# Kernel optimization log

Measured on AMD Instinct MI355X. Metric: run time of the kernel, lower is better.

## Reference

```python
import jax, jax.numpy as jnp
import numpy as np

B, N, E = 8, 5000, 80000
NODE_IN, EDGE_IN, HIDDEN, EMBED = 32, 16, 128, 64


def setup_inputs() -> dict:
    key = jax.random.key(0)
    ks = jax.random.split(key, 20)
    g = lambda k, shape: jax.random.normal(k, shape, dtype=jnp.float32) * 0.05
    return {
        "node_x": jax.random.normal(ks[0], (B, N, NODE_IN), dtype=jnp.float32),
        "edge_attr": jax.random.normal(ks[1], (B, E, EDGE_IN), dtype=jnp.float32),
        "edge_index": jax.random.randint(ks[2], (2, E), 0, N),
        "ln_node_g": jnp.ones((NODE_IN,), jnp.float32),
        "ln_node_b": jnp.zeros((NODE_IN,), jnp.float32),
        "ln_edge_g": jnp.ones((EDGE_IN,), jnp.float32),
        "ln_edge_b": jnp.zeros((EDGE_IN,), jnp.float32),
        "gat0_W": g(ks[3], (NODE_IN, HIDDEN)),
        "gat0_We": g(ks[4], (EDGE_IN, HIDDEN)),
        "gat0_asrc": g(ks[5], (HIDDEN,)),
        "gat0_adst": g(ks[6], (HIDDEN,)),
        "gat0_ae": g(ks[7], (HIDDEN,)),
        "gat0_b": jnp.zeros((HIDDEN,), jnp.float32),
        "gat1_W": g(ks[8], (HIDDEN, EMBED)),
        "gat1_We": g(ks[9], (EDGE_IN, EMBED)),
        "gat1_asrc": g(ks[10], (EMBED,)),
        "gat1_adst": g(ks[11], (EMBED,)),
        "gat1_ae": g(ks[12], (EMBED,)),
        "gat1_b": jnp.zeros((EMBED,), jnp.float32),
        "mlp_W1": g(ks[13], (4 * EMBED + EDGE_IN, HIDDEN)),
        "mlp_b1": jnp.zeros((HIDDEN,), jnp.float32),
        "mlp_W2": g(ks[14], (HIDDEN, 1)),
        "mlp_b2": jnp.zeros((1,), jnp.float32),
    }


def _layernorm(x, g, b, eps=1e-5):
    mu = x.mean(-1, keepdims=True)
    var = ((x - mu) ** 2).mean(-1, keepdims=True)
    return (x - mu) * jax.lax.rsqrt(var + eps) * g + b


def _gat_layer(x, efeat, src, dst, W, We, asrc, adst, ae, b, nseg):
    # Single-head GATConv with edge features: attention logits from src/dst/edge projections,
    # segment-softmax over incoming edges per destination node, weighted-sum aggregation.
    h = x @ W                      # [nseg, out]
    he = efeat @ We                # [num_edges, out]
    logits = jax.nn.leaky_relu(
        (h[src] * asrc).sum(-1) + (h[dst] * adst).sum(-1) + (he * ae).sum(-1), 0.2)
    m = jax.ops.segment_max(logits, dst, num_segments=nseg)
    m = jnp.where(jnp.isfinite(m), m, 0.0)
    ex = jnp.exp(logits - m[dst])
    denom = jax.ops.segment_sum(ex, dst, num_segments=nseg)
    alpha = ex / (denom[dst] + 1e-16)
    return jax.ops.segment_sum(alpha[:, None] * h[src], dst, num_segments=nseg) + b


def reference(node_x, edge_attr, edge_index, ln_node_g, ln_node_b, ln_edge_g, ln_edge_b,
              gat0_W, gat0_We, gat0_asrc, gat0_adst, gat0_ae, gat0_b,
              gat1_W, gat1_We, gat1_asrc, gat1_adst, gat1_ae, gat1_b,
              mlp_W1, mlp_b1, mlp_W2, mlp_b2):
    nx = _layernorm(node_x, ln_node_g, ln_node_b)
    ea = _layernorm(edge_attr, ln_edge_g, ln_edge_b)
    # Batched graph: offset shared edge_index per graph.
    xf = nx.reshape(B * N, NODE_IN)
    ef = ea.reshape(B * E, EDGE_IN)
    offs = jnp.arange(B) * N
    ei = (edge_index[:, None, :] + offs[None, :, None]).reshape(2, B * E)
    src, dst = ei[0], ei[1]
    batch_vec = jnp.repeat(jnp.arange(B), N)
    # GAT encoder: layer 0 (ELU) then final projection to embed.
    h = jax.nn.elu(_gat_layer(xf, ef, src, dst, gat0_W, gat0_We, gat0_asrc, gat0_adst, gat0_ae, gat0_b, B * N))
    node_emb = _gat_layer(h, ef, src, dst, gat1_W, gat1_We, gat1_asrc, gat1_adst, gat1_ae, gat1_b, B * N)
    # Global context: concat(mean, max) pooling per graph -> [B, 2*EMBED]
    mean_pool = jax.ops.segment_sum(node_emb, batch_vec, num_segments=B) / N
    max_pool = jax.ops.segment_max(node_emb, batch_vec, num_segments=B)
    ctx = jnp.concatenate([mean_pool, max_pool], axis=-1)
    # Per-edge gather-concat + MLP
    edge_emb = jnp.concatenate([node_emb[src], node_emb[dst], ef, ctx[batch_vec[src]]], axis=-1)
    hm = jax.nn.relu(edge_emb @ mlp_W1 + mlp_b1)
    q = (hm @ mlp_W2 + mlp_b2).squeeze(-1)
    return q.reshape(B, E)
```

## Files before the change

### kernel.cpp

```cpp
#include <hip/hip_runtime.h>
#include <cmath>

#define BB 8
#define NN 5000
#define EE 80000
#define NODE_IN 32
#define EDGE_IN 16
#define HIDDEN 128
#define EMBED 64
#define BN (BB*NN)
#define BE (BB*EE)

typedef unsigned short u16;
typedef __attribute__((ext_vector_type(8))) __bf16 bf16x8;
typedef __attribute__((ext_vector_type(4))) float f32x4;

__device__ __forceinline__ float waveSum(float v){
  #pragma unroll
  for(int o=32;o;o>>=1) v += __shfl_xor(v,o);
  return v;
}
__device__ __forceinline__ float waveMax(float v){
  #pragma unroll
  for(int o=32;o;o>>=1) v = fmaxf(v,__shfl_xor(v,o));
  return v;
}
__device__ __forceinline__ int rlanei(int v, int l){
  return __builtin_amdgcn_readlane(v, l);
}
__device__ __forceinline__ float rlanef(float v, int l){
  return __uint_as_float(__builtin_amdgcn_readlane(__float_as_uint(v), l));
}
__device__ __forceinline__ unsigned pack_bf2(float a0, float a1){
  unsigned u0 = __float_as_uint(a0), u1 = __float_as_uint(a1);
  unsigned r0 = (u0 + 0x7fffu + ((u0>>16)&1u)) >> 16;
  unsigned r1 = (u1 + 0x7fffu + ((u1>>16)&1u)) & 0xffff0000u;
  return r0 | r1;
}
__device__ __forceinline__ u16 bf16r(float x){
  unsigned u = __float_as_uint(x);
  return (u16)((u + 0x7fffu + ((u>>16)&1u)) >> 16);
}
__device__ __forceinline__ float bflo(unsigned h){ return __uint_as_float(h<<16); }
__device__ __forceinline__ float bfhi(unsigned h){ return __uint_as_float(h & 0xffff0000u); }
__device__ __forceinline__ bf16x8 ld8_or_zero(const u16* p, bool pred){
  uint4 v = pred ? *(const uint4*)p : make_uint4(0u,0u,0u,0u);
  return *(bf16x8*)&v;
}

__launch_bounds__(256)
__global__ void k_prep(const float* We0, const float* ae0,
                       const float* We1, const float* ae1,
                       const float* W1g, const float* asrc1, const float* adst1,
                       const float* mlpW1,
                       float* wae, float* ws1, float* wd1,
                       u16* BT1u, u16* BT2u, u16* AT1e){
  int t = threadIdx.x;
  if(blockIdx.x == 0){
    if(t < 16){
      float a = 0.f;
      for(int k=0;k<HIDDEN;k++) a += We0[t*HIDDEN+k]*ae0[k];
      wae[t] = a;
    } else if(t < 32){
      int j = t-16;
      float a = 0.f;
      for(int k=0;k<EMBED;k++) a += We1[j*EMBED+k]*ae1[k];
      wae[16+j] = a;
    }
    if(t < 128){
      float s = 0.f, d = 0.f;
      for(int k=0;k<EMBED;k++){
        float w = W1g[t*EMBED+k];
        s += w*asrc1[k];
        d += w*adst1[k];
      }
      ws1[t] = s; wd1[t] = d;
    }
    for(int i=t; i<2048; i+=256){
      int o = i >> 4, k = i & 15;
      AT1e[o*16 + k] = bf16r(mlpW1[(128+k)*HIDDEN + o]);
    }
  } else {
    #pragma unroll
    for(int ii=0; ii<6; ii++){
      int idx = (blockIdx.x-1)*1536 + ii*256 + t;
      if(idx < 8192){
        int c = idx >> 7, k = idx & 127;
        BT1u[c*136 + k] = bf16r(W1g[k*EMBED + c]);
      } else {
        int i2 = idx - 8192;
        int d = i2 >> 6, j = i2 & 63;
        float v = (d < 128) ? mlpW1[j*HIDDEN + d] : mlpW1[(64+j)*HIDDEN + (d-128)];
        BT2u[d*72 + j] = bf16r(v);
      }
    }
  }
}

__launch_bounds__(256)
__global__ void k_node(const float* __restrict__ x, const float* __restrict__ g,
                       const float* __restrict__ bb, const float* __restrict__ W,
                       const float* __restrict__ asrc, const float* __restrict__ adst,
                       unsigned* __restrict__ H0u, float* __restrict__ S0o, float* __restrict__ D0o){
  int t = threadIdx.x;
  int w = t>>6, lane = t&63;
  float w0r[NODE_IN], w1r[NODE_IN];
  #pragma unroll
  for(int j=0;j<NODE_IN;j++){
    w0r[j] = W[j*HIDDEN + 2*lane];
    w1r[j] = W[j*HIDDEN + 2*lane + 1];
  }
  float gl = (lane<NODE_IN)? g[lane] : 0.f;
  float bl = (lane<NODE_IN)? bb[lane] : 0.f;
  float asl0 = asrc[2*lane], asl1 = asrc[2*lane+1];
  float adl0 = adst[2*lane], adl1 = adst[2*lane+1];
  for(int nb = blockIdx.x; nb < BN/4; nb += gridDim.x){
    int n = nb*4 + w;
    float xv = (lane<NODE_IN)? x[n*NODE_IN+lane] : 0.f;
    float s  = waveSum(xv);
    float s2 = waveSum(xv*xv);
    float mu = s*(1.f/NODE_IN);
    float var = s2*(1.f/NODE_IN) - mu*mu;
    float inv = 1.0f / sqrtf(var + 1e-5f);
    float nx = (lane<NODE_IN)? ((xv-mu)*inv*gl + bl) : 0.f;
    float a0=0.f, a1=0.f;
    #pragma unroll
    for(int j=0;j<NODE_IN;j++){
      float r = rlanef(nx, j);
      a0 += r*w0r[j];
      a1 += r*w1r[j];
    }
    H0u[(size_t)n*64 + lane] = pack_bf2(a0, a1);
    float sv = waveSum(a0*asl0 + a1*asl1);
    float dv = waveSum(a0*adl0 + a1*adl1);
    if(lane==0){ S0o[n]=sv; D0o[n]=dv; }
  }
}

__launch_bounds__(256)
__global__ void k_edge(const float* __restrict__ ein, const float* __restrict__ g,
                       const float* __restrict__ bb, const float* __restrict__ wae,
                       const int* __restrict__ EPOS,
                       u16* __restrict__ EAb, float* __restrict__ E0p, float* __restrict__ E1p){
  int ge = blockIdx.x*256 + threadIdx.x;
  int b = ge / EE, e = ge - b*EE;
  int gp = b*EE + EPOS[e];
  float v[EDGE_IN];
  const float4* p = (const float4*)(ein + (size_t)ge*EDGE_IN);
  float4 q0=p[0], q1=p[1], q2=p[2], q3=p[3];
  v[0]=q0.x; v[1]=q0.y; v[2]=q0.z; v[3]=q0.w;
  v[4]=q1.x; v[5]=q1.y; v[6]=q1.z; v[7]=q1.w;
  v[8]=q2.x; v[9]=q2.y; v[10]=q2.z; v[11]=q2.w;
  v[12]=q3.x; v[13]=q3.y; v[14]=q3.z; v[15]=q3.w;
  float s=0.f, s2=0.f;
  #pragma unroll
  for(int j=0;j<EDGE_IN;j++){ s += v[j]; s2 += v[j]*v[j]; }
  float mu = s*(1.f/EDGE_IN);
  float var = s2*(1.f/EDGE_IN) - mu*mu;
  float inv = 1.0f / sqrtf(var + 1e-5f);
  float e0=0.f, e1=0.f;
  #pragma unroll
  for(int j=0;j<EDGE_IN;j++){
    float nv = (v[j]-mu)*inv*g[j] + bb[j];
    v[j] = nv;
    e0 += nv*wae[j];
    e1 += nv*wae[16+j];
  }
  uint4 w0 = make_uint4(pack_bf2(v[0],v[1]), pack_bf2(v[2],v[3]),
                        pack_bf2(v[4],v[5]), pack_bf2(v[6],v[7]));
  uint4 w1 = make_uint4(pack_bf2(v[8],v[9]), pack_bf2(v[10],v[11]),
                        pack_bf2(v[12],v[13]), pack_bf2(v[14],v[15]));
  uint4* q = (uint4*)&EAb[(size_t)gp*16];
  q[0] = w0; q[1] = w1;
  E0p[gp]=e0; E1p[gp]=e1;
}

__global__ void k_count(const int* __restrict__ ei, int* __restrict__ cnt){
  int e = blockIdx.x*256 + threadIdx.x;
  if(e < EE) atomicAdd(&cnt[ei[EE+e]], 1);
}

__launch_bounds__(1024)
__global__ void k_scan(int* __restrict__ off, int* __restrict__ cur){
  __shared__ int part[1024];
  int t = threadIdx.x;
  int loc[5]; int s=0;
  int base = t*5;
  #pragma unroll
  for(int k=0;k<5;k++){ int idx=base+k; int c=(idx<NN)? cur[idx]:0; loc[k]=s; s+=c; }
  part[t]=s;
  __syncthreads();
  for(int o=1;o<1024;o<<=1){
    int v = (t>=o)? part[t-o] : 0;
    __syncthreads();
    part[t] += v;
    __syncthreads();
  }
  int pre = (t>0)? part[t-1] : 0;
  #pragma unroll
  for(int k=0;k<5;k++){
    int idx=base+k;
    if(idx<NN){ int o2 = pre+loc[k]; off[idx]=o2; cur[idx]=o2; }
  }
  if(t==0) off[NN] = EE;
}

__global__ void k_fill(const int* __restrict__ ei, int* __restrict__ cur,
                       int* __restrict__ csrc, int* __restrict__ cdst,
                       int* __restrict__ ceid, int* __restrict__ epos){
  int e = blockIdx.x*256 + threadIdx.x;
  if(e < EE){
    int d = ei[EE+e];
    int pos = atomicAdd(&cur[d], 1);
    csrc[pos] = ei[e];
    cdst[pos] = d;
    ceid[pos] = e;
    epos[e] = pos;
  }
}

__launch_bounds__(256)
__global__ void k_gat0(const unsigned* __restrict__ H0u, const float* __restrict__ S0,
                       const float* __restrict__ D0, const float* __restrict__ E0p,
                       const int* __restrict__ off, const int* __restrict__ csrc,
                       const float* __restrict__ bias,
                       const float* __restrict__ WS1, const float* __restrict__ WD1,
                       unsigned* __restrict__ HELUu, float* __restrict__ S1o, float* __restrict__ D1o){
  int t = threadIdx.x, w = t>>6, lane = t&63;
  int b = blockIdx.x & 7, c = blockIdx.x >> 3;
  int n = c*4 + w;
  int gid = b*NN + n;
  int base = off[n], deg = off[n+1]-base;
  const float* s0b = S0 + b*NN;
  const float* e0b = E0p + b*EE;
  const unsigned* h0b = H0u + (size_t)b*NN*64;
  float dv = D0[gid];
  float acc0=0.f, acc1=0.f;
  if(deg > 0){
    if(deg <= 64){
      float lg = -INFINITY; int sidx = 0;
      if(lane < deg){
        sidx = csrc[base+lane];
        float xx = s0b[sidx] + dv + e0b[base+lane];
        lg = xx>0.f ? xx : 0.2f*xx;
      }
      float m = waveMax(lg);
      float ex = (lane<deg)? __expf(lg-m) : 0.f;
      float den = waveSum(ex);
      float al = ex / (den + 1e-16f);
      int nb8 = (deg+7)>>3;
      for(int b8=0;b8<nb8;b8++){
        int i0 = b8*8;
        int ss[8]; float aa[8]; unsigned hh[8];
        #pragma unroll
        for(int kk=0;kk<8;kk++){ ss[kk]=rlanei(sidx, i0+kk); aa[kk]=rlanef(al, i0+kk); }
        #pragma unroll
        for(int kk=0;kk<8;kk++){ hh[kk]=h0b[ss[kk]*64 + lane]; }
        #pragma unroll
        for(int kk=0;kk<8;kk++){ acc0 += aa[kk]*bflo(hh[kk]); acc1 += aa[kk]*bfhi(hh[kk]); }
      }
    } else {
      float m = -INFINITY;
      for(int i=lane;i<deg;i+=64){
        float xx = s0b[csrc[base+i]] + dv + e0b[base+i];
        xx = xx>0.f ? xx : 0.2f*xx;
        m = fmaxf(m, xx);
      }
      m = waveMax(m);
      float den = 0.f;
      for(int i=lane;i<deg;i+=64){
        float xx = s0b[csrc[base+i]] + dv + e0b[base+i];
        xx = xx>0.f ? xx : 0.2f*xx;
        den += __expf(xx-m);
      }
      den = waveSum(den) + 1e-16f;
      for(int i=0;i<deg;i++){
        int s = csrc[base+i];
        float xx = s0b[s] + dv + e0b[base+i];
        xx = xx>0.f ? xx : 0.2f*xx;
        float a = __expf(xx-m)/den;
        unsigned h = h0b[s*64 + lane];
        acc0 += a*bflo(h);
        acc1 += a*bfhi(h);
      }
    }
  }
  float2 bi = *(const float2*)&bias[2*lane];
  float v0 = acc0 + bi.x;
  float v1 = acc1 + bi.y;
  v0 = v0>0.f ? v0 : (__expf(v0)-1.f);
  v1 = v1>0.f ? v1 : (__expf(v1)-1.f);
  HELUu[(size_t)gid*64 + lane] = pack_bf2(v0, v1);
  float2 wsv = *(const float2*)&WS1[2*lane];
  float2 wdv = *(const float2*)&WD1[2*lane];
  float sv1 = waveSum(v0*wsv.x + v1*wsv.y);
  float dv1 = waveSum(v0*wdv.x + v1*wdv.y);
  if(lane==0){ S1o[gid]=sv1; D1o[gid]=dv1; }
}

__launch_bounds__(256)
__global__ void k_h1(const unsigned* __restrict__ HELUu, const u16* __restrict__ BT1,
                     u16* __restrict__ H1u){
  __shared__ u16 Ald[64*136];
  __shared__ u16 Bld[64*136];
  int t = threadIdx.x;
  int n0 = blockIdx.x*64;
  #pragma unroll
  for(int ii=0; ii<4; ii++){
    int c2 = ii*256 + t;
    int r = c2 >> 4, q = c2 & 15;
    *(uint4*)&Ald[r*136 + q*8] = ((const uint4*)(HELUu + (size_t)(n0+r)*64))[q];
  }
  for(int i=t; i<1088; i+=256) ((uint4*)Bld)[i] = ((const uint4*)BT1)[i];
  __syncthreads();
  int w = t>>6, lane = t&63;
  int lo = lane & 15, hi = lane >> 4;
  f32x4 acc0 = {0.f,0.f,0.f,0.f}, acc1 = acc0, acc2 = acc0, acc3 = acc0;
  #pragma unroll
  for(int ks=0; ks<4; ks++){
    bf16x8 a = *(const bf16x8*)&Ald[(w*16+lo)*136 + ks*32 + hi*8];
    bf16x8 b0 = *(const bf16x8*)&Bld[(0*16+lo)*136 + ks*32 + hi*8];
    bf16x8 b1 = *(const bf16x8*)&Bld[(1*16+lo)*136 + ks*32 + hi*8];
    bf16x8 b2 = *(const bf16x8*)&Bld[(2*16+lo)*136 + ks*32 + hi*8];
    bf16x8 b3 = *(const bf16x8*)&Bld[(3*16+lo)*136 + ks*32 + hi*8];
    acc0 = __builtin_amdgcn_mfma_f32_16x16x32_bf16(a, b0, acc0, 0,0,0);
    acc1 = __builtin_amdgcn_mfma_f32_16x16x32_bf16(a, b1, acc1, 0,0,0);
    acc2 = __builtin_amdgcn_mfma_f32_16x16x32_bf16(a, b2, acc2, 0,0,0);
    acc3 = __builtin_amdgcn_mfma_f32_16x16x32_bf16(a, b3, acc3, 0,0,0);
  }
  int rowb = n0 + w*16 + hi*4;
  #pragma unroll
  for(int r=0;r<4;r++){
    H1u[(size_t)(rowb+r)*64 +  0 + lo] = bf16r(acc0[r]);
    H1u[(size_t)(rowb+r)*64 + 16 + lo] = bf16r(acc1[r]);
    H1u[(size_t)(rowb+r)*64 + 32 + lo] = bf16r(acc2[r]);
    H1u[(size_t)(rowb+r)*64 + 48 + lo] = bf16r(acc3[r]);
  }
}

__launch_bounds__(256)
__global__ void k_gat1(const u16* __restrict__ H1u, const float* __restrict__ S1,
                       const float* __restrict__ D1, const float* __restrict__ E1p,
                       const int* __restrict__ off, const int* __restrict__ csrc,
                       const float* __restrict__ bias, float* __restrict__ out){
  int t = threadIdx.x, w = t>>6, lane = t&63;
  int b = blockIdx.x & 7, c = blockIdx.x >> 3;
  int n = c*4 + w;
  int gid = b*NN + n;
  int base = off[n], deg = off[n+1]-base;
  const float* s1b = S1 + b*NN;
  const float* e1b = E1p + b*EE;
  const u16* h1b = H1u + (size_t)b*NN*64;
  float dv = D1[gid];
  float acc = 0.f;
  if(deg > 0){
    if(deg <= 64){
      float lg = -INFINITY; int sidx = 0;
      if(lane < deg){
        sidx = csrc[base+lane];
        float xx = s1b[sidx] + dv + e1b[base+lane];
        lg = xx>0.f ? xx : 0.2f*xx;
      }
      float m = waveMax(lg);
      float ex = (lane<deg)? __expf(lg-m) : 0.f;
      float den = waveSum(ex);
      float al = ex / (den + 1e-16f);
      int nb8 = (deg+7)>>3;
      for(int b8=0;b8<nb8;b8++){
        int i0 = b8*8;
        int ss[8]; float aa[8]; unsigned hh[8];
        #pragma unroll
        for(int kk=0;kk<8;kk++){ ss[kk]=rlanei(sidx, i0+kk); aa[kk]=rlanef(al, i0+kk); }
        #pragma unroll
        for(int kk=0;kk<8;kk++){ hh[kk]=h1b[ss[kk]*64 + lane]; }
        #pragma unroll
        for(int kk=0;kk<8;kk++){ acc += aa[kk]*__uint_as_float(hh[kk]<<16); }
      }
    } else {
      float m = -INFINITY;
      for(int i=lane;i<deg;i+=64){
        float xx = s1b[csrc[base+i]] + dv + e1b[base+i];
        xx = xx>0.f ? xx : 0.2f*xx;
        m = fmaxf(m, xx);
      }
      m = waveMax(m);
      float den = 0.f;
      for(int i=lane;i<deg;i+=64){
        float xx = s1b[csrc[base+i]] + dv + e1b[base+i];
        xx = xx>0.f ? xx : 0.2f*xx;
        den += __expf(xx-m);
      }
      den = waveSum(den) + 1e-16f;
      for(int i=0;i<deg;i++){
        int s = csrc[base+i];
        float xx = s1b[s] + dv + e1b[base+i];
        xx = xx>0.f ? xx : 0.2f*xx;
        float a = __expf(xx-m)/den;
        acc += a*__uint_as_float(((unsigned)h1b[s*64 + lane])<<16);
      }
    }
  }
  out[(size_t)gid*EMBED + lane] = acc + bias[lane];
}

__launch_bounds__(256)
__global__ void k_pool(const float* __restrict__ EMBp, float* __restrict__ PSUM,
                       float* __restrict__ PMAX){
  int blk = blockIdx.x & 31, b = blockIdx.x >> 5;
  int t = threadIdx.x;
  int dim = t & 63, chunk = t >> 6;
  int n0 = blk*157, n1 = n0+157 < NN ? n0+157 : NN;
  float sm = 0.f, mx = -INFINITY;
  for(int n=n0+chunk; n<n1; n+=4){
    float v = EMBp[((size_t)(b*NN+n))*EMBED + dim];
    sm += v; mx = fmaxf(mx, v);
  }
  __shared__ float ssum[256], smax[256];
  ssum[t]=sm; smax[t]=mx;
  __syncthreads();
  if(t < 64){
    float S = ssum[t]+ssum[t+64]+ssum[t+128]+ssum[t+192];
    float M = fmaxf(fmaxf(smax[t],smax[t+64]), fmaxf(smax[t+128],smax[t+192]));
    PSUM[(b*32+blk)*64 + t] = S;
    PMAX[(b*32+blk)*64 + t] = M;
  }
}

__launch_bounds__(128)
__global__ void k_ctxp(const float* __restrict__ PSUM, const float* __restrict__ PMAX,
                       const float* __restrict__ W1, const float* __restrict__ b1,
                       float* __restrict__ CTXP){
  int b = blockIdx.x, c = threadIdx.x;
  __shared__ float cl[128];
  if(c < 64){
    float S = 0.f;
    for(int k=0;k<32;k++) S += PSUM[(b*32+k)*64 + c];
    cl[c] = S*(1.f/NN);
  } else {
    float M = -INFINITY;
    for(int k=0;k<32;k++) M = fmaxf(M, PMAX[(b*32+k)*64 + (c-64)]);
    cl[c] = M;
  }
  __syncthreads();
  float a = b1[c];
  for(int j=0;j<128;j++) a += cl[j]*W1[(144+j)*HIDDEN + c];
  CTXP[b*128+c] = a;
}

__launch_bounds__(256)
__global__ void k_psd(const float* __restrict__ EMB, const u16* __restrict__ BT2,
                      const float* __restrict__ CTXP,
                      u16* __restrict__ PSu, u16* __restrict__ PDu){
  __shared__ u16 Ald[64*72];
  __shared__ u16 Bld[256*72];
  int t = threadIdx.x;
  int n0 = blockIdx.x*64;
  #pragma unroll
  for(int ii=0; ii<2; ii++){
    int c2 = ii*256 + t;
    int r = c2 >> 3, q = c2 & 7;
    const float4* src = (const float4*)(EMB + (size_t)(n0+r)*EMBED + q*8);
    float4 f0 = src[0], f1 = src[1];
    uint4 pk = make_uint4(pack_bf2(f0.x,f0.y), pack_bf2(f0.z,f0.w),
                          pack_bf2(f1.x,f1.y), pack_bf2(f1.z,f1.w));
    *(uint4*)&Ald[r*72 + q*8] = pk;
  }
  for(int i=t; i<2304; i+=256) ((uint4*)Bld)[i] = ((const uint4*)BT2)[i];
  __syncthreads();
  int w = t>>6, lane = t&63;
  int lo = lane & 15, hi = lane >> 4;
  f32x4 acc[16];
  #pragma unroll
  for(int i=0;i<16;i++) acc[i] = (f32x4){0.f,0.f,0.f,0.f};
  #pragma unroll
  for(int ks=0; ks<2; ks++){
    bf16x8 a = *(const bf16x8*)&Ald[(w*16+lo)*72 + ks*32 + hi*8];
    #pragma unroll
    for(int nt=0; nt<16; nt++){
      bf16x8 b = *(const bf16x8*)&Bld[(nt*16+lo)*72 + ks*32 + hi*8];
      acc[nt] = __builtin_amdgcn_mfma_f32_16x16x32_bf16(a, b, acc[nt], 0,0,0);
    }
  }
  int rowb = n0 + w*16 + hi*4;
  #pragma unroll
  for(int r=0;r<4;r++){
    int row = rowb + r;
    int bg = row / NN;
    const float* cp = CTXP + bg*128;
    #pragma unroll
    for(int nt=0; nt<16; nt++){
      int dim = (nt & 7)*16 + lo;
      u16 u = bf16r(acc[nt][r] + 0.5f*cp[dim]);
      if(nt < 8) PSu[(size_t)row*HIDDEN + dim] = u;
      else       PDu[(size_t)row*HIDDEN + dim] = u;
    }
  }
}

__launch_bounds__(256)
__global__ void k_final(const u16* __restrict__ EAb, const int* __restrict__ csrc,
                        const int* __restrict__ cdst, const int* __restrict__ ceid,
                        const u16* __restrict__ PS, const u16* __restrict__ PD,
                        const u16* __restrict__ AT1e,
                        const float* __restrict__ W2, const float* __restrict__ b2,
                        float* __restrict__ out){
  __shared__ unsigned ldsPS[4][16][66];
  int t = threadIdx.x, w = t>>6, lane = t&63;
  int lo = lane & 15, hi = lane >> 4;
  int b = blockIdx.x & 7, c = blockIdx.x >> 3;
  int pg = c*64 + w*16;
  bf16x8 afr[8];
  #pragma unroll
  for(int mt=0;mt<8;mt++) afr[mt] = ld8_or_zero(&AT1e[(mt*16+lo)*16 + hi*8], hi<2);
  float4 w2r[8];
  #pragma unroll
  for(int mt=0;mt<8;mt++) w2r[mt] = *(const float4*)&W2[mt*16 + hi*4];
  float bias2 = b2[0];
  const unsigned* PSb32 = (const unsigned*)(PS + (size_t)b*NN*HIDDEN);
  const u16* PDb = PD + (size_t)b*NN*HIDDEN;
  int s = csrc[pg + lo];
  int d = cdst[pg + lo];
  unsigned vs[16];
  #pragma unroll
  for(int k=0;k<16;k++){
    int sk = rlanei(s, k);
    vs[k] = PSb32[(size_t)sk*64 + lane];
  }
  const u16* qr = PDb + (size_t)d*HIDDEN + hi*4;
  uint2 pdv[8];
  #pragma unroll
  for(int mt=0;mt<8;mt++) pdv[mt] = *(const uint2*)(qr + mt*16);
  bf16x8 bfr = ld8_or_zero(&EAb[((size_t)b*EE + pg + lo)*16 + hi*8], hi<2);
  #pragma unroll
  for(int k=0;k<16;k++) ldsPS[w][k][lane] = vs[k];
  f32x4 acc[8];
  #pragma unroll
  for(int mt=0;mt<8;mt++){
    f32x4 z = {0.f,0.f,0.f,0.f};
    acc[mt] = __builtin_amdgcn_mfma_f32_16x16x32_bf16(afr[mt], bfr, z, 0,0,0);
  }
  float qp = 0.f;
  #pragma unroll
  for(int mt=0;mt<8;mt++){
    uint2 psv = *(const uint2*)&ldsPS[w][lo][hi*2 + mt*8];
    float h0 = acc[mt][0] + bflo(psv.x) + bflo(pdv[mt].x);
    float h1 = acc[mt][1] + bfhi(psv.x) + bfhi(pdv[mt].x);
    float h2 = acc[mt][2] + bflo(psv.y) + bflo(pdv[mt].y);
    float h3 = acc[mt][3] + bfhi(psv.y) + bfhi(pdv[mt].y);
    qp += fmaxf(h0,0.f)*w2r[mt].x + fmaxf(h1,0.f)*w2r[mt].y
        + fmaxf(h2,0.f)*w2r[mt].z + fmaxf(h3,0.f)*w2r[mt].w;
  }
  qp += __shfl_xor(qp, 16);
  qp += __shfl_xor(qp, 32);
  if(lane < 16){
    int ev = ceid[pg + lane];
    out[(size_t)b*EE + ev] = qp + bias2;
  }
}

extern "C" void kernel_launch(void* const* d_in, const int* in_sizes, int n_in,
                              void* d_out, int out_size, void* d_ws, size_t ws_size,
                              hipStream_t stream) {
  const float* node_x   = (const float*)d_in[0];
  const float* edge_attr= (const float*)d_in[1];
  const int*   edge_idx = (const int*)d_in[2];
  const float* ln_ng    = (const float*)d_in[3];
  const float* ln_nb    = (const float*)d_in[4];
  const float* ln_eg    = (const float*)d_in[5];
  const float* ln_eb    = (const float*)d_in[6];
  const float* g0_W     = (const float*)d_in[7];
  const float* g0_We    = (const float*)d_in[8];
  const float* g0_asrc  = (const float*)d_in[9];
  const float* g0_adst  = (const float*)d_in[10];
  const float* g0_ae    = (const float*)d_in[11];
  const float* g0_b     = (const float*)d_in[12];
  const float* g1_W     = (const float*)d_in[13];
  const float* g1_We    = (const float*)d_in[14];
  const float* g1_asrc  = (const float*)d_in[15];
  const float* g1_adst  = (const float*)d_in[16];
  const float* g1_ae    = (const float*)d_in[17];
  const float* g1_b     = (const float*)d_in[18];
  const float* mlp_W1   = (const float*)d_in[19];
  const float* mlp_b1   = (const float*)d_in[20];
  const float* mlp_W2   = (const float*)d_in[21];
  const float* mlp_b2   = (const float*)d_in[22];
  float* out = (float*)d_out;

  float* ws   = (float*)d_ws;
  float* EAp  = ws;
  float* E0p  = EAp  + (size_t)BE*EDGE_IN;
  float* E1p  = E0p  + BE;
  float* H0   = E1p  + BE;
  float* HELU = H0   + (size_t)BN*HIDDEN;
  float* H1   = HELU + (size_t)BN*HIDDEN;
  float* EMBa = H1   + (size_t)BN*EMBED;
  float* S0   = EMBa + (size_t)BN*EMBED;
  float* D0   = S0 + BN;
  float* S1   = D0 + BN;
  float* D1   = S1 + BN;
  float* CTX  = D1 + BN;
  float* CTXP = CTX + 1024;
  float* WAE  = CTXP + 1024;
  int* CSR_OFF = (int*)(WAE + 32);
  int* CSR_CUR = CSR_OFF + (NN+4);
  int* CSR_SRC = CSR_CUR + NN;
  int* CSR_DST = CSR_SRC + EE;
  int* CSR_EID = CSR_DST + EE;
  int* EPOS    = CSR_EID + EE;
  float* WS1   = (float*)(EPOS + EE);
  float* WD1   = WS1 + 128;
  u16* BT1u    = (u16*)(WD1 + 128);
  u16* BT2u    = BT1u + 64*136;
  float* PSUM  = (float*)(BT2u + 256*72);
  float* PMAX  = PSUM + 256*64;
  u16* AT1e    = (u16*)(PMAX + 256*64);
  u16* EAb16      = (u16*)EAp;
  unsigned* H0u   = (unsigned*)H0;
  unsigned* HELUu = (unsigned*)HELU;
  u16*      H1u   = (u16*)H1;
  u16* PS = (u16*)H0;
  u16* PD = (u16*)HELU;

  hipMemsetAsync(CSR_CUR, 0, NN*sizeof(int), stream);
  k_prep<<<17, 256, 0, stream>>>(g0_We, g0_ae, g1_We, g1_ae, g1_W, g1_asrc, g1_adst,
                                 mlp_W1, WAE, WS1, WD1, BT1u, BT2u, AT1e);
  k_count<<<(EE+255)/256, 256, 0, stream>>>(edge_idx, CSR_CUR);
  k_scan<<<1, 1024, 0, stream>>>(CSR_OFF, CSR_CUR);
  k_fill<<<(EE+255)/256, 256, 0, stream>>>(edge_idx, CSR_CUR, CSR_SRC, CSR_DST, CSR_EID, EPOS);
  k_node<<<1024, 256, 0, stream>>>(node_x, ln_ng, ln_nb, g0_W, g0_asrc, g0_adst, H0u, S0, D0);
  k_edge<<<BE/256, 256, 0, stream>>>(edge_attr, ln_eg, ln_eb, WAE, EPOS, EAb16, E0p, E1p);
  k_gat0<<<BN/4, 256, 0, stream>>>(H0u, S0, D0, E0p, CSR_OFF, CSR_SRC, g0_b, WS1, WD1, HELUu, S1, D1);
  k_h1<<<BN/64, 256, 0, stream>>>(HELUu, BT1u, H1u);
  k_gat1<<<BN/4, 256, 0, stream>>>(H1u, S1, D1, E1p, CSR_OFF, CSR_SRC, g1_b, EMBa);
  k_pool<<<256, 256, 0, stream>>>(EMBa, PSUM, PMAX);
  k_ctxp<<<BB, 128, 0, stream>>>(PSUM, PMAX, mlp_W1, mlp_b1, CTXP);
  k_psd<<<BN/64, 256, 0, stream>>>(EMBa, BT2u, CTXP, PS, PD);
  k_final<<<BE/64, 256, 0, stream>>>(EAb16, CSR_SRC, CSR_DST, CSR_EID, PS, PD, AT1e, mlp_W2, mlp_b2, out);
}
```

Before: 313.4 us.

## Precompute source logit terms per edge, fuse pooling into gat1, double k_final work

The source-node attention term S0[src] is folded into the per-edge logit buffer in k_edge. A new k_lg1 kernel does the same for layer 1, so the GAT kernels no longer do an indirect S lookup per edge. Pooling moves into k_gat1 through block reductions and global atomics, with sum as float atomicAdd and max through an order-preserving uint key, which removes the k_pool kernel and its partial buffers. k_final now handles 32 edges per wave instead of 16 to amortise the fragment loads, at the cost of an extra kernel launch, atomic contention and nondeterministic float summation order.

```diff
diff --git a/kernel.cpp b/kernel.cpp
--- a/kernel.cpp
+++ b/kernel.cpp
@@ -46,6 +46,13 @@
 __device__ __forceinline__ bf16x8 ld8_or_zero(const u16* p, bool pred){
   uint4 v = pred ? *(const uint4*)p : make_uint4(0u,0u,0u,0u);
   return *(bf16x8*)&v;
+}
+__device__ __forceinline__ unsigned fkey(float x){
+  unsigned s = __float_as_uint(x);
+  return (s & 0x80000000u) ? ~s : (s | 0x80000000u);
+}
+__device__ __forceinline__ float funkey(unsigned k){
+  return __uint_as_float((k & 0x80000000u) ? (k & 0x7fffffffu) : ~k);
 }
 
 __launch_bounds__(256)
@@ -140,8 +147,9 @@
 __launch_bounds__(256)
 __global__ void k_edge(const float* __restrict__ ein, const float* __restrict__ g,
                        const float* __restrict__ bb, const float* __restrict__ wae,
-                       const int* __restrict__ EPOS,
-                       u16* __restrict__ EAb, float* __restrict__ E0p, float* __restrict__ E1p){
+                       const int* __restrict__ EPOS, const int* __restrict__ ei,
+                       const float* __restrict__ S0,
+                       u16* __restrict__ EAb, float* __restrict__ LG0p, float* __restrict__ E1p){
   int ge = blockIdx.x*256 + threadIdx.x;
   int b = ge / EE, e = ge - b*EE;
   int gp = b*EE + EPOS[e];
@@ -172,7 +180,8 @@
                         pack_bf2(v[12],v[13]), pack_bf2(v[14],v[15]));
   uint4* q = (uint4*)&EAb[(size_t)gp*16];
   q[0] = w0; q[1] = w1;
-  E0p[gp]=e0; E1p[gp]=e1;
+  LG0p[gp] = e0 + S0[b*NN + ei[e]];
+  E1p[gp]  = e1;
 }
 
 __global__ void k_count(const int* __restrict__ ei, int* __restrict__ cnt){
@@ -220,8 +229,8 @@
 }
 
 __launch_bounds__(256)
-__global__ void k_gat0(const unsigned* __restrict__ H0u, const float* __restrict__ S0,
-                       const float* __restrict__ D0, const float* __restrict__ E0p,
+__global__ void k_gat0(const unsigned* __restrict__ H0u, const float* __restrict__ D0,
+                       const float* __restrict__ LG0p,
                        const int* __restrict__ off, const int* __restrict__ csrc,
                        const float* __restrict__ bias,
                        const float* __restrict__ WS1, const float* __restrict__ WD1,
@@ -231,8 +240,7 @@
   int n = c*4 + w;
   int gid = b*NN + n;
   int base = off[n], deg = off[n+1]-base;
-  const float* s0b = S0 + b*NN;
-  const float* e0b = E0p + b*EE;
+  const float* lg0b = LG0p + b*EE;
   const unsigned* h0b = H0u + (size_t)b*NN*64;
   float dv = D0[gid];
   float acc0=0.f, acc1=0.f;
@@ -241,7 +249,7 @@
       float lg = -INFINITY; int sidx = 0;
       if(lane < deg){
         sidx = csrc[base+lane];
-        float xx = s0b[sidx] + dv + e0b[base+lane];
+        float xx = lg0b[base+lane] + dv;
         lg = xx>0.f ? xx : 0.2f*xx;
       }
       float m = waveMax(lg);
@@ -262,21 +270,21 @@
     } else {
       float m = -INFINITY;
       for(int i=lane;i<deg;i+=64){
-        float xx = s0b[csrc[base+i]] + dv + e0b[base+i];
+        float xx = lg0b[base+i] + dv;
         xx = xx>0.f ? xx : 0.2f*xx;
         m = fmaxf(m, xx);
       }
       m = waveMax(m);
       float den = 0.f;
       for(int i=lane;i<deg;i+=64){
-        float xx = s0b[csrc[base+i]] + dv + e0b[base+i];
+        float xx = lg0b[base+i] + dv;
         xx = xx>0.f ? xx : 0.2f*xx;
         den += __expf(xx-m);
       }
       den = waveSum(den) + 1e-16f;
       for(int i=0;i<deg;i++){
         int s = csrc[base+i];
-        float xx = s0b[s] + dv + e0b[base+i];
+        float xx = lg0b[base+i] + dv;
         xx = xx>0.f ? xx : 0.2f*xx;
         float a = __expf(xx-m)/den;
         unsigned h = h0b[s*64 + lane];
@@ -298,6 +306,13 @@
   if(lane==0){ S1o[gid]=sv1; D1o[gid]=dv1; }
 }
 
+__global__ void k_lg1(const float* __restrict__ S1, const int* __restrict__ csrc,
+                      float* __restrict__ LG1){
+  int p = blockIdx.x*256 + threadIdx.x;
+  int b = p / EE, pp = p - b*EE;
+  LG1[p] += S1[b*NN + csrc[pp]];
+}
+
 __launch_bounds__(256)
 __global__ void k_h1(const unsigned* __restrict__ HELUu, const u16* __restrict__ BT1,
                      u16* __restrict__ H1u){
@@ -339,17 +354,19 @@
 }
 
 __launch_bounds__(256)
-__global__ void k_gat1(const u16* __restrict__ H1u, const float* __restrict__ S1,
-                       const float* __restrict__ D1, const float* __restrict__ E1p,
+__global__ void k_gat1(const u16* __restrict__ H1u, const float* __restrict__ D1,
+                       const float* __restrict__ LG1,
                        const int* __restrict__ off, const int* __restrict__ csrc,
-                       const float* __restrict__ bias, float* __restrict__ out){
+                       const float* __restrict__ bias, float* __restrict__ out,
+                       float* __restrict__ PSUM, unsigned* __restrict__ PMAXu){
+  __shared__ float lsum[4][64];
+  __shared__ unsigned lkey[4][64];
   int t = threadIdx.x, w = t>>6, lane = t&63;
   int b = blockIdx.x & 7, c = blockIdx.x >> 3;
   int n = c*4 + w;
   int gid = b*NN + n;
   int base = off[n], deg = off[n+1]-base;
-  const float* s1b = S1 + b*NN;
-  const float* e1b = E1p + b*EE;
+  const float* e1b = LG1 + b*EE;
   const u16* h1b = H1u + (size_t)b*NN*64;
   float dv = D1[gid];
   float acc = 0.f;
@@ -358,7 +375,7 @@
       float lg = -INFINITY; int sidx = 0;
       if(lane < deg){
         sidx = csrc[base+lane];
-        float xx = s1b[sidx] + dv + e1b[base+lane];
+        float xx = e1b[base+lane] + dv;
         lg = xx>0.f ? xx : 0.2f*xx;
       }
       float m = waveMax(lg);
@@ -379,68 +396,48 @@
     } else {
       float m = -INFINITY;
       for(int i=lane;i<deg;i+=64){
-        float xx = s1b[csrc[base+i]] + dv + e1b[base+i];
+        float xx = e1b[base+i] + dv;
         xx = xx>0.f ? xx : 0.2f*xx;
         m = fmaxf(m, xx);
       }
       m = waveMax(m);
       float den = 0.f;
       for(int i=lane;i<deg;i+=64){
-        float xx = s1b[csrc[base+i]] + dv + e1b[base+i];
+        float xx = e1b[base+i] + dv;
         xx = xx>0.f ? xx : 0.2f*xx;
         den += __expf(xx-m);
       }
       den = waveSum(den) + 1e-16f;
       for(int i=0;i<deg;i++){
         int s = csrc[base+i];
-        float xx = s1b[s] + dv + e1b[base+i];
+        float xx = e1b[base+i] + dv;
         xx = xx>0.f ? xx : 0.2f*xx;
         float a = __expf(xx-m)/den;
         acc += a*__uint_as_float(((unsigned)h1b[s*64 + lane])<<16);
       }
     }
   }
-  out[(size_t)gid*EMBED + lane] = acc + bias[lane];
-}
-
-__launch_bounds__(256)
-__global__ void k_pool(const float* __restrict__ EMBp, float* __restrict__ PSUM,
-                       float* __restrict__ PMAX){
-  int blk = blockIdx.x & 31, b = blockIdx.x >> 5;
-  int t = threadIdx.x;
-  int dim = t & 63, chunk = t >> 6;
-  int n0 = blk*157, n1 = n0+157 < NN ? n0+157 : NN;
-  float sm = 0.f, mx = -INFINITY;
-  for(int n=n0+chunk; n<n1; n+=4){
-    float v = EMBp[((size_t)(b*NN+n))*EMBED + dim];
-    sm += v; mx = fmaxf(mx, v);
-  }
-  __shared__ float ssum[256], smax[256];
-  ssum[t]=sm; smax[t]=mx;
+  float o = acc + bias[lane];
+  out[(size_t)gid*EMBED + lane] = o;
+  lsum[w][lane] = o;
+  lkey[w][lane] = fkey(o);
   __syncthreads();
   if(t < 64){
-    float S = ssum[t]+ssum[t+64]+ssum[t+128]+ssum[t+192];
-    float M = fmaxf(fmaxf(smax[t],smax[t+64]), fmaxf(smax[t+128],smax[t+192]));
-    PSUM[(b*32+blk)*64 + t] = S;
-    PMAX[(b*32+blk)*64 + t] = M;
+    float S = lsum[0][t]+lsum[1][t]+lsum[2][t]+lsum[3][t];
+    unsigned K = max(max(lkey[0][t],lkey[1][t]), max(lkey[2][t],lkey[3][t]));
+    atomicAdd(&PSUM[b*64+t], S);
+    atomicMax(&PMAXu[b*64+t], K);
   }
 }
 
 __launch_bounds__(128)
-__global__ void k_ctxp(const float* __restrict__ PSUM, const float* __restrict__ PMAX,
+__global__ void k_ctxp(const float* __restrict__ PSUM, const unsigned* __restrict__ PMAXu,
                        const float* __restrict__ W1, const float* __restrict__ b1,
                        float* __restrict__ CTXP){
   int b = blockIdx.x, c = threadIdx.x;
   __shared__ float cl[128];
-  if(c < 64){
-    float S = 0.f;
-    for(int k=0;k<32;k++) S += PSUM[(b*32+k)*64 + c];
-    cl[c] = S*(1.f/NN);
-  } else {
-    float M = -INFINITY;
-    for(int k=0;k<32;k++) M = fmaxf(M, PMAX[(b*32+k)*64 + (c-64)]);
-    cl[c] = M;
-  }
+  if(c < 64) cl[c] = PSUM[b*64+c] * (1.f/NN);
+  else       cl[c] = funkey(PMAXu[b*64 + (c-64)]);
   __syncthreads();
   float a = b1[c];
   for(int j=0;j<128;j++) a += cl[j]*W1[(144+j)*HIDDEN + c];
@@ -508,7 +505,7 @@
   int t = threadIdx.x, w = t>>6, lane = t&63;
   int lo = lane & 15, hi = lane >> 4;
   int b = blockIdx.x & 7, c = blockIdx.x >> 3;
-  int pg = c*64 + w*16;
+  int pg = c*128 + w*32;
   bf16x8 afr[8];
   #pragma unroll
   for(int mt=0;mt<8;mt++) afr[mt] = ld8_or_zero(&AT1e[(mt*16+lo)*16 + hi*8], hi<2);
@@ -518,43 +515,47 @@
   float bias2 = b2[0];
   const unsigned* PSb32 = (const unsigned*)(PS + (size_t)b*NN*HIDDEN);
   const u16* PDb = PD + (size_t)b*NN*HIDDEN;
-  int s = csrc[pg + lo];
-  int d = cdst[pg + lo];
-  unsigned vs[16];
-  #pragma unroll
-  for(int k=0;k<16;k++){
-    int sk = rlanei(s, k);
-    vs[k] = PSb32[(size_t)sk*64 + lane];
-  }
-  const u16* qr = PDb + (size_t)d*HIDDEN + hi*4;
-  uint2 pdv[8];
-  #pragma unroll
-  for(int mt=0;mt<8;mt++) pdv[mt] = *(const uint2*)(qr + mt*16);
-  bf16x8 bfr = ld8_or_zero(&EAb[((size_t)b*EE + pg + lo)*16 + hi*8], hi<2);
-  #pragma unroll
-  for(int k=0;k<16;k++) ldsPS[w][k][lane] = vs[k];
-  f32x4 acc[8];
-  #pragma unroll
-  for(int mt=0;mt<8;mt++){
-    f32x4 z = {0.f,0.f,0.f,0.f};
-    acc[mt] = __builtin_amdgcn_mfma_f32_16x16x32_bf16(afr[mt], bfr, z, 0,0,0);
-  }
-  float qp = 0.f;
-  #pragma unroll
-  for(int mt=0;mt<8;mt++){
-    uint2 psv = *(const uint2*)&ldsPS[w][lo][hi*2 + mt*8];
-    float h0 = acc[mt][0] + bflo(psv.x) + bflo(pdv[mt].x);
-    float h1 = acc[mt][1] + bfhi(psv.x) + bfhi(pdv[mt].x);
-    float h2 = acc[mt][2] + bflo(psv.y) + bflo(pdv[mt].y);
-    float h3 = acc[mt][3] + bfhi(psv.y) + bfhi(pdv[mt].y);
-    qp += fmaxf(h0,0.f)*w2r[mt].x + fmaxf(h1,0.f)*w2r[mt].y
-        + fmaxf(h2,0.f)*w2r[mt].z + fmaxf(h3,0.f)*w2r[mt].w;
-  }
-  qp += __shfl_xor(qp, 16);
-  qp += __shfl_xor(qp, 32);
-  if(lane < 16){
-    int ev = ceid[pg + lane];
-    out[(size_t)b*EE + ev] = qp + bias2;
+  int sv = (lane<32)? csrc[pg+lane] : 0;
+  #pragma unroll
+  for(int g=0; g<2; g++){
+    int pgg = pg + g*16;
+    unsigned vs[16];
+    #pragma unroll
+    for(int k=0;k<16;k++){
+      int sk = rlanei(sv, g*16+k);
+      vs[k] = PSb32[(size_t)sk*64 + lane];
+    }
+    int d = cdst[pgg + lo];
+    const u16* qr = PDb + (size_t)d*HIDDEN + hi*4;
+    uint2 pdv[8];
+    #pragma unroll
+    for(int mt=0;mt<8;mt++) pdv[mt] = *(const uint2*)(qr + mt*16);
+    bf16x8 bfr = ld8_or_zero(&EAb[((size_t)b*EE + pgg + lo)*16 + hi*8], hi<2);
+    #pragma unroll
+    for(int k=0;k<16;k++) ldsPS[w][k][lane] = vs[k];
+    f32x4 acc[8];
+    #pragma unroll
+    for(int mt=0;mt<8;mt++){
+      f32x4 z = {0.f,0.f,0.f,0.f};
+      acc[mt] = __builtin_amdgcn_mfma_f32_16x16x32_bf16(afr[mt], bfr, z, 0,0,0);
+    }
+    float qp = 0.f;
+    #pragma unroll
+    for(int mt=0;mt<8;mt++){
+      uint2 psv = *(const uint2*)&ldsPS[w][lo][hi*2 + mt*8];
+      float h0 = acc[mt][0] + bflo(psv.x) + bflo(pdv[mt].x);
+      float h1 = acc[mt][1] + bfhi(psv.x) + bfhi(pdv[mt].x);
+      float h2 = acc[mt][2] + bflo(psv.y) + bflo(pdv[mt].y);
+      float h3 = acc[mt][3] + bfhi(psv.y) + bfhi(pdv[mt].y);
+      qp += fmaxf(h0,0.f)*w2r[mt].x + fmaxf(h1,0.f)*w2r[mt].y
+          + fmaxf(h2,0.f)*w2r[mt].z + fmaxf(h3,0.f)*w2r[mt].w;
+    }
+    qp += __shfl_xor(qp, 16);
+    qp += __shfl_xor(qp, 32);
+    if(lane < 16){
+      int ev = ceid[pgg + lane];
+      out[(size_t)b*EE + ev] = qp + bias2;
+    }
   }
 }
 
@@ -588,8 +589,8 @@
 
   float* ws   = (float*)d_ws;
   float* EAp  = ws;
-  float* E0p  = EAp  + (size_t)BE*EDGE_IN;
-  float* E1p  = E0p  + BE;
+  float* LG0p = EAp  + (size_t)BE*EDGE_IN;
+  float* E1p  = LG0p + BE;
   float* H0   = E1p  + BE;
   float* HELU = H0   + (size_t)BN*HIDDEN;
   float* H1   = HELU + (size_t)BN*HIDDEN;
@@ -612,8 +613,8 @@
   u16* BT1u    = (u16*)(WD1 + 128);
   u16* BT2u    = BT1u + 64*136;
   float* PSUM  = (float*)(BT2u + 256*72);
-  float* PMAX  = PSUM + 256*64;
-  u16* AT1e    = (u16*)(PMAX + 256*64);
+  unsigned* PMAXu = (unsigned*)(PSUM + 512);
+  u16* AT1e    = (u16*)(PMAXu + 512);
   u16* EAb16      = (u16*)EAp;
   unsigned* H0u   = (unsigned*)H0;
   unsigned* HELUu = (unsigned*)HELU;
@@ -622,18 +623,20 @@
   u16* PD = (u16*)HELU;
 
   hipMemsetAsync(CSR_CUR, 0, NN*sizeof(int), stream);
+  hipMemsetAsync(PSUM, 0, 1024*sizeof(int), stream);
   k_prep<<<17, 256, 0, stream>>>(g0_We, g0_ae, g1_We, g1_ae, g1_W, g1_asrc, g1_adst,
                                  mlp_W1, WAE, WS1, WD1, BT1u, BT2u, AT1e);
   k_count<<<(EE+255)/256, 256, 0, stream>>>(edge_idx, CSR_CUR);
   k_scan<<<1, 1024, 0, stream>>>(CSR_OFF, CSR_CUR);
   k_fill<<<(EE+255)/256, 256, 0, stream>>>(edge_idx, CSR_CUR, CSR_SRC, CSR_DST, CSR_EID, EPOS);
   k_node<<<1024, 256, 0, stream>>>(node_x, ln_ng, ln_nb, g0_W, g0_asrc, g0_adst, H0u, S0, D0);
-  k_edge<<<BE/256, 256, 0, stream>>>(edge_attr, ln_eg, ln_eb, WAE, EPOS, EAb16, E0p, E1p);
-  k_gat0<<<BN/4, 256, 0, stream>>>(H0u, S0, D0, E0p, CSR_OFF, CSR_SRC, g0_b, WS1, WD1, HELUu, S1, D1);
+  k_edge<<<BE/256, 256, 0, stream>>>(edge_attr, ln_eg, ln_eb, WAE, EPOS, edge_idx, S0,
+                                     EAb16, LG0p, E1p);
+  k_gat0<<<BN/4, 256, 0, stream>>>(H0u, D0, LG0p, CSR_OFF, CSR_SRC, g0_b, WS1, WD1, HELUu, S1, D1);
+  k_lg1<<<BE/256, 256, 0, stream>>>(S1, CSR_SRC, E1p);
   k_h1<<<BN/64, 256, 0, stream>>>(HELUu, BT1u, H1u);
-  k_gat1<<<BN/4, 256, 0, stream>>>(H1u, S1, D1, E1p, CSR_OFF, CSR_SRC, g1_b, EMBa);
-  k_pool<<<256, 256, 0, stream>>>(EMBa, PSUM, PMAX);
-  k_ctxp<<<BB, 128, 0, stream>>>(PSUM, PMAX, mlp_W1, mlp_b1, CTXP);
+  k_gat1<<<BN/4, 256, 0, stream>>>(H1u, D1, E1p, CSR_OFF, CSR_SRC, g1_b, EMBa, PSUM, PMAXu);
+  k_ctxp<<<BB, 128, 0, stream>>>(PSUM, PMAXu, mlp_W1, mlp_b1, CTXP);
   k_psd<<<BN/64, 256, 0, stream>>>(EMBa, BT2u, CTXP, PS, PD);
-  k_final<<<BE/64, 256, 0, stream>>>(EAb16, CSR_SRC, CSR_DST, CSR_EID, PS, PD, AT1e, mlp_W2, mlp_b2, out);
-}
+  k_final<<<BE/128, 256, 0, stream>>>(EAb16, CSR_SRC, CSR_DST, CSR_EID, PS, PD, AT1e, mlp_W2, mlp_b2, out);
+}
```

After: 332.6 us. 6.1% more time.
